# Performance work log

Measured on AMD Instinct MI355X. Metric: run time of the kernel, lower is better.

Reference implementation:

```python
import jax, jax.numpy as jnp
import numpy as np

B, N, H, D, N_HEADS = 8, 2048, 1024, 1, 8
SCALE = H / N_HEADS  # 128.0 ; note: NOT sqrt, faithful to source


def _linear(x, w, b):
    # torch nn.Linear: y = x @ W^T + b ; w: [out, in]
    return jnp.einsum('bnh,oh->bno', x, w) + b


def setup_inputs() -> dict:
    key = jax.random.key(0)
    ks = jax.random.split(key, 18)
    s = 0.02
    inp = {
        'node_t': jax.random.normal(ks[0], (B, N, H), dtype=jnp.float32),
        'node_next': jax.random.normal(ks[1], (B, N, H), dtype=jnp.float32),
        'WQ_w': s * jax.random.normal(ks[2], (H, H), dtype=jnp.float32),
        'WQ_b': s * jax.random.normal(ks[3], (H,), dtype=jnp.float32),
        'WK_w': s * jax.random.normal(ks[4], (H, H), dtype=jnp.float32),
        'WK_b': s * jax.random.normal(ks[5], (H,), dtype=jnp.float32),
        'WV_w': s * jax.random.normal(ks[6], (H, H), dtype=jnp.float32),
        'WV_b': s * jax.random.normal(ks[7], (H,), dtype=jnp.float32),
        'WO_w': s * jax.random.normal(ks[8], (H, H), dtype=jnp.float32),
        'WO_b': s * jax.random.normal(ks[9], (H,), dtype=jnp.float32),
        'WE_w': s * jax.random.normal(ks[10], (H, H), dtype=jnp.float32),
        'WE_b': s * jax.random.normal(ks[11], (H,), dtype=jnp.float32),
        'WN_w': s * jax.random.normal(ks[12], (H, H), dtype=jnp.float32),
        'WN_b': s * jax.random.normal(ks[13], (H,), dtype=jnp.float32),
        'WA_w': s * jax.random.normal(ks[14], (D, H), dtype=jnp.float32),
        'WA_b': s * jax.random.normal(ks[15], (D,), dtype=jnp.float32),
    }
    return inp


def reference(node_t, node_next, WQ_w, WQ_b, WK_w, WK_b, WV_w, WV_b,
              WO_w, WO_b, WE_w, WE_b, WN_w, WN_b, WA_w, WA_b):
    Q = _linear(node_t, WQ_w, WQ_b)       # [B,N,H]
    K = _linear(node_next, WK_w, WK_b)    # [B,N,H]
    V = _linear(node_next, WV_w, WV_b)    # [B,N,H]
    att = jnp.einsum('bih,bkh->bik', Q, K)  # [B,N,N]
    # torch nn.Softmax() with no dim on a 3-D tensor -> legacy dim=0 (batch axis)
    att = jax.nn.softmax(att / SCALE, axis=0)
    # einsum('bnn,bnd->bnd') uses only the diagonal att[b,n,n]
    diag = jnp.einsum('bnn->bn', att)  # [B,N]
    av = diag[:, :, None] * V          # [B,N,H]
    h = jax.nn.gelu(_linear(av, WO_w, WO_b), approximate=False)  # exact erf GELU
    A_t = _linear(node_t, WE_w, WE_b) + _linear(h, WN_w, WN_b)   # [B,N,H]
    A_t = _linear(A_t, WA_w, WA_b)     # [B,N,1]
    return jnp.squeeze(A_t, axis=-1)   # [B,N]
```

## Files before the change

### kernel.cpp

```cpp
#include <hip/hip_runtime.h>
#include <cstdint>
#include <cstddef>


typedef __attribute__((ext_vector_type(8))) short bfx8;
typedef __attribute__((ext_vector_type(4))) short s16x4;
typedef __attribute__((ext_vector_type(4))) float f32x4;

#define N_SEQ 2048
#define M_TOT 16384
#define NT 16

__device__ __forceinline__ unsigned short f2bf(float f) {
  unsigned int u = __float_as_uint(f);
  return (unsigned short)((u + 0x7fffu + ((u >> 16) & 1u)) >> 16);
}
__device__ __forceinline__ float bf2f(short s) {
  return __uint_as_float(((unsigned int)(unsigned short)s) << 16);
}
__device__ __forceinline__ float gelu_exact(float g) {
  return 0.5f * g * (1.0f + erff(g * 0.70710678118654752f));
}
__device__ __forceinline__ void gload16(const void* g, void* l) {
  __builtin_amdgcn_global_load_lds(
      (const __attribute__((address_space(1))) unsigned int*)g,
      (__attribute__((address_space(3))) unsigned int*)(unsigned int)(uintptr_t)l,
      16, 0, 0);
}
__device__ __forceinline__ float blk_sum(float v, float* red, int t) {
#pragma unroll
  for (int o = 32; o > 0; o >>= 1) v += __shfl_down(v, o, 64);
  __syncthreads();
  if ((t & 63) == 0) red[t >> 6] = v;
  __syncthreads();
  return red[0] + red[1] + red[2] + red[3];
}

__global__ __launch_bounds__(256) void colred_kernel(
    const float* __restrict__ WE, const float* __restrict__ WN,
    const float* __restrict__ WQ, const float* __restrict__ WK,
    const float* __restrict__ wa, const float* __restrict__ bQ,
    const float* __restrict__ bK, const float* __restrict__ WEb,
    const float* __restrict__ WNb, const float* __restrict__ WAb,
    float* __restrict__ vE, float* __restrict__ vN,
    float* __restrict__ uQ, float* __restrict__ uK,
    float* __restrict__ c0, float* __restrict__ c1) {
  int y = blockIdx.y;
  if (y < 4) {
    const float* M = y == 0 ? WE : y == 1 ? WN : y == 2 ? WQ : WK;
    const float* wv = (y < 2) ? wa : (y == 2 ? bK : bQ);
    float* dst = y == 0 ? vE : y == 1 ? vN : y == 2 ? uQ : uK;
    int h = blockIdx.x * 256 + threadIdx.x;
    float a = 0.f;
    for (int o = 0; o < 1024; ++o) a += wv[o] * M[(size_t)o * 1024 + h];
    dst[h] = a;
  } else if (blockIdx.x < 2) {
    int t = threadIdx.x;
    float a = 0.f;
    if (blockIdx.x == 0)
      for (int i = t; i < 1024; i += 256) a += wa[i] * (WEb[i] + WNb[i]);
    else
      for (int i = t; i < 1024; i += 256) a += bQ[i] * bK[i];
#pragma unroll
    for (int o = 32; o > 0; o >>= 1) a += __shfl_down(a, o, 64);
    __shared__ float r4[4];
    if ((t & 63) == 0) r4[t >> 6] = a;
    __syncthreads();
    if (t == 0) {
      float tot = r4[0] + r4[1] + r4[2] + r4[3];
      if (blockIdx.x == 0) c0[0] = tot + WAb[0];
      else c1[0] = tot;
    }
  }
}

__global__ __launch_bounds__(256) void rowdot_kernel(
    const float* __restrict__ WO, const float* __restrict__ bV,
    float* __restrict__ bvw) {
  int r = blockIdx.x, t = threadIdx.x;
  __shared__ float red[4];
  float4 wv = ((const float4*)(WO + (size_t)r * 1024))[t];
  float4 bv = ((const float4*)bV)[t];
  float a = wv.x * bv.x + wv.y * bv.y + wv.z * bv.z + wv.w * bv.w;
  float tot = blk_sum(a, red, t);
  if (t == 0) bvw[r] = tot;
}

__global__ __launch_bounds__(256) void cvt_wT_kernel(
    const float* __restrict__ WQ, const float* __restrict__ WK,
    const float* __restrict__ WV, const float* __restrict__ WO,
    short* __restrict__ wqT, short* __restrict__ wkT,
    short* __restrict__ wvT, short* __restrict__ wo) {
  int bi = blockIdx.x, bj = blockIdx.y, z = blockIdx.z, t = threadIdx.x;
  const float* src = z == 0 ? WQ : z == 1 ? WK : z == 2 ? WV : WO;
  if (z == 3) {
#pragma unroll
    for (int i = 0; i < 16; ++i) {
      int lin = i * 256 + t, r = lin >> 6, c = lin & 63;
      size_t idx = (size_t)(bi * 64 + r) * 1024 + bj * 64 + c;
      wo[idx] = (short)f2bf(src[idx]);
    }
    return;
  }
  __shared__ short tile[64][65];
  short* dst = z == 0 ? wqT : z == 1 ? wkT : wvT;
#pragma unroll
  for (int i = 0; i < 16; ++i) {
    int lin = i * 256 + t, r = lin >> 6, c = lin & 63;
    tile[r][c] = (short)f2bf(src[(size_t)(bi * 64 + r) * 1024 + bj * 64 + c]);
  }
  __syncthreads();
#pragma unroll
  for (int i = 0; i < 16; ++i) {
    int lin = i * 256 + t, r = lin >> 6, c = lin & 63;
    dst[(size_t)(bj * 64 + r) * 1024 + bi * 64 + c] = tile[c][r];
  }
}

__global__ __launch_bounds__(128) void cvt_nn_kernel(
    const float* __restrict__ nn, const float* __restrict__ uK,
    short* __restrict__ xn, float* __restrict__ xk) {
  int row = blockIdx.x, t = threadIdx.x;
  const float* src = nn + (size_t)row * 1024 + t * 8;
  float4 v0 = *(const float4*)src;
  float4 v1 = *(const float4*)(src + 4);
  bfx8 o;
  o[0] = (short)f2bf(v0.x); o[1] = (short)f2bf(v0.y);
  o[2] = (short)f2bf(v0.z); o[3] = (short)f2bf(v0.w);
  o[4] = (short)f2bf(v1.x); o[5] = (short)f2bf(v1.y);
  o[6] = (short)f2bf(v1.z); o[7] = (short)f2bf(v1.w);
  *(bfx8*)(xn + (size_t)row * 1024 + t * 8) = o;
  const float4* uv = (const float4*)(uK + t * 8);
  float4 e0 = uv[0], e1 = uv[1];
  float a = v0.x * e0.x + v0.y * e0.y + v0.z * e0.z + v0.w * e0.w +
            v1.x * e1.x + v1.y * e1.y + v1.z * e1.z + v1.w * e1.w;
#pragma unroll
  for (int off = 32; off > 0; off >>= 1) a += __shfl_down(a, off, 64);
  __shared__ float r2[2];
  if ((t & 63) == 0) r2[t >> 6] = a;
  __syncthreads();
  if (t == 0) xk[row] = r2[0] + r2[1];
}

__global__ __launch_bounds__(256) void gemm_pre(
    const short* __restrict__ A0, const short* __restrict__ B0,
    short* __restrict__ D0, const short* __restrict__ A1,
    const short* __restrict__ B1, short* __restrict__ D1) {
  const short* A = blockIdx.z ? A1 : A0;
  const short* B = blockIdx.z ? B1 : B0;
  short* D = blockIdx.z ? D1 : D0;
  __shared__ short sA[128 * 64];
  __shared__ short sB[128 * 64];
  int tid = threadIdx.x, lane = tid & 63, w = tid >> 6;
  int wm = w >> 1, wn = w & 1;
  int bx = blockIdx.x, by = blockIdx.y;
  f32x4 acc[4][4] = {};
  int lrow = lane & 15, lk = (lane >> 4) * 8;
  int srow = lane >> 3, scol = (lane & 7) * 8;
  const short* Ag = A + (size_t)by * 128 * 1024;
  const short* Bg = B + (size_t)bx * 128 * 1024;
  for (int k0 = 0; k0 < 1024; k0 += 64) {
#pragma unroll
    for (int i = 0; i < 4; ++i) {
      int c = w * 4 + i;
      gload16(Ag + (size_t)(c * 8 + srow) * 1024 + k0 + scol, sA + c * 512);
      gload16(Bg + (size_t)(c * 8 + srow) * 1024 + k0 + scol, sB + c * 512);
    }
    __syncthreads();
#pragma unroll
    for (int kk = 0; kk < 64; kk += 32) {
      bfx8 af[4], bfr[4];
#pragma unroll
      for (int mi = 0; mi < 4; ++mi)
        af[mi] = *(const bfx8*)(sA + (wm * 64 + mi * 16 + lrow) * 64 + kk + lk);
#pragma unroll
      for (int nj = 0; nj < 4; ++nj)
        bfr[nj] = *(const bfx8*)(sB + (wn * 64 + nj * 16 + lrow) * 64 + kk + lk);
#pragma unroll
      for (int mi = 0; mi < 4; ++mi)
#pragma unroll
        for (int nj = 0; nj < 4; ++nj)
          acc[mi][nj] = __builtin_amdgcn_mfma_f32_16x16x32_bf16(
              af[mi], bfr[nj], acc[mi][nj], 0, 0, 0);
    }
    __syncthreads();
  }
  int r0 = by * 128 + wm * 64, cb = bx * 128 + wn * 64;
#pragma unroll
  for (int mi = 0; mi < 4; ++mi)
#pragma unroll
    for (int nj = 0; nj < 4; ++nj) {
      int col = cb + nj * 16 + lrow;
#pragma unroll
      for (int r = 0; r < 4; ++r) {
        int row = r0 + mi * 16 + (lane >> 4) * 4 + r;
        D[(size_t)row * 1024 + col] = (short)f2bf(acc[mi][nj][r]);
      }
    }
}

__global__ __launch_bounds__(512, 2) void gemm_main(
    const short* __restrict__ A, const short* __restrict__ Bf,
    const float* __restrict__ bias2, const float* __restrict__ nodet,
    const float* __restrict__ vE, float* __restrict__ sPart,
    float* __restrict__ xePart, short* __restrict__ vw) {
  __shared__ short sA[2][16384];
  __shared__ short sB[2][16384];
  int tid = threadIdx.x;
  int lane = tid & 63, w = tid >> 6;
  int wm = w >> 2, wn = w & 3;
  int wg = blockIdx.x;
  int work = (wg & 7) * 64 + (wg >> 3);
  int by = work >> 3, bx = work & 7;
  int lrow = lane & 15, g = lane >> 4;
  int sw0 = g ^ (lrow & 7);
  int sg = (lane & 7) ^ (lane >> 3);
  const short* Agt = A + ((size_t)(by * 256 + w * 32 + (lane >> 3))) * 1024 + sg * 8;
  const short* Bgt = Bf + ((size_t)(bx * 256 + w * 32 + (lane >> 3))) * 1024 + sg * 8;

  f32x4 acc[8][4] = {};

  auto stage = [&](int buf, int kt) {
    const short* ag = Agt + kt * 64;
    const short* bg = Bgt + kt * 64;
    short* la = &sA[buf][w * 2048];
    short* lb = &sB[buf][w * 2048];
#pragma unroll
    for (int i = 0; i < 4; ++i) {
      gload16(ag + i * 8192, la + i * 512);
      gload16(bg + i * 8192, lb + i * 512);
    }
  };

  stage(0, 0);
  int arow = wm * 128 + lrow;
  int brow = wn * 64 + lrow;
  for (int kt = 0; kt < NT; ++kt) {
    int cur = kt & 1;
    if (kt + 1 < NT) {
      stage(cur ^ 1, kt + 1);
      asm volatile("s_waitcnt vmcnt(8)" ::: "memory");
    } else {
      asm volatile("s_waitcnt vmcnt(0)" ::: "memory");
    }
    __builtin_amdgcn_sched_barrier(0);
    __builtin_amdgcn_s_barrier();
    __builtin_amdgcn_sched_barrier(0);

    const short* sa = &sA[cur][0];
    const short* sb = &sB[cur][0];
    bfx8 bq[4][2];
#pragma unroll
    for (int nj = 0; nj < 4; ++nj) {
      bq[nj][0] = *(const bfx8*)(sb + (brow + nj * 16) * 64 + sw0 * 8);
      bq[nj][1] = *(const bfx8*)(sb + (brow + nj * 16) * 64 + (sw0 ^ 4) * 8);
    }
    bfx8 a0 = *(const bfx8*)(sa + (arow + 0 * 16) * 64 + sw0 * 8);
    bfx8 a1 = *(const bfx8*)(sa + (arow + 0 * 16) * 64 + (sw0 ^ 4) * 8);
    bfx8 a2 = *(const bfx8*)(sa + (arow + 1 * 16) * 64 + sw0 * 8);
    bfx8 a3 = *(const bfx8*)(sa + (arow + 1 * 16) * 64 + (sw0 ^ 4) * 8);
#pragma unroll
    for (int q = 0; q < 4; ++q) {
      bfx8 n0 = a0, n1 = a1, n2 = a2, n3 = a3;
      if (q < 3) {
        n0 = *(const bfx8*)(sa + (arow + (2 * q + 2) * 16) * 64 + sw0 * 8);
        n1 = *(const bfx8*)(sa + (arow + (2 * q + 2) * 16) * 64 + (sw0 ^ 4) * 8);
        n2 = *(const bfx8*)(sa + (arow + (2 * q + 3) * 16) * 64 + sw0 * 8);
        n3 = *(const bfx8*)(sa + (arow + (2 * q + 3) * 16) * 64 + (sw0 ^ 4) * 8);
      }
      __builtin_amdgcn_s_setprio(1);
#pragma unroll
      for (int nj = 0; nj < 4; ++nj) {
        acc[2 * q][nj] = __builtin_amdgcn_mfma_f32_16x16x32_bf16(
            a0, bq[nj][0], acc[2 * q][nj], 0, 0, 0);
        acc[2 * q][nj] = __builtin_amdgcn_mfma_f32_16x16x32_bf16(
            a1, bq[nj][1], acc[2 * q][nj], 0, 0, 0);
        acc[2 * q + 1][nj] = __builtin_amdgcn_mfma_f32_16x16x32_bf16(
            a2, bq[nj][0], acc[2 * q + 1][nj], 0, 0, 0);
        acc[2 * q + 1][nj] = __builtin_amdgcn_mfma_f32_16x16x32_bf16(
            a3, bq[nj][1], acc[2 * q + 1][nj], 0, 0, 0);
      }
      __builtin_amdgcn_s_setprio(0);
      __builtin_amdgcn_sched_barrier(0);
      __builtin_amdgcn_s_barrier();
      __builtin_amdgcn_sched_barrier(0);
      a0 = n0; a1 = n1; a2 = n2; a3 = n3;
    }
  }

  int row0 = by * 256 + wm * 128;
  int cb = bx * 256 + wn * 64;
  if (bx < 4) {
    float bias_nj[4], ve_nj[4];
#pragma unroll
    for (int nj = 0; nj < 4; ++nj) {
      bias_nj[nj] = bias2[cb + nj * 16 + lrow];
      ve_nj[nj] = vE[cb + nj * 16 + lrow];
    }
    int px = bx * 4 + wn;
#pragma unroll
    for (int mi = 0; mi < 8; ++mi) {
#pragma unroll
      for (int r = 0; r < 4; ++r) {
        int row = row0 + mi * 16 + g * 4 + r;
        const float* xr = nodet + (size_t)row * 1024;
        float v = 0.f, v2 = 0.f;
#pragma unroll
        for (int nj = 0; nj < 4; ++nj) {
          float xv = xr[cb + nj * 16 + lrow];
          v += (acc[mi][nj][r] + bias_nj[nj]) * xv;
          v2 += ve_nj[nj] * xv;
        }
        v += __shfl_xor(v, 1, 64);   v2 += __shfl_xor(v2, 1, 64);
        v += __shfl_xor(v, 2, 64);   v2 += __shfl_xor(v2, 2, 64);
        v += __shfl_xor(v, 4, 64);   v2 += __shfl_xor(v2, 4, 64);
        v += __shfl_xor(v, 8, 64);   v2 += __shfl_xor(v2, 8, 64);
        if (lrow == 0) {
          sPart[(size_t)row * 16 + px] = v;
          xePart[(size_t)row * 16 + px] = v2;
        }
      }
    }
  } else {
#pragma unroll
    for (int mi = 0; mi < 8; ++mi)
#pragma unroll
      for (int nj = 0; nj < 4; ++nj) {
        int colv = cb - 1024 + nj * 16 + lrow;
        float bv = bias2[1024 + colv];
#pragma unroll
        for (int r = 0; r < 4; ++r) {
          int row = row0 + mi * 16 + g * 4 + r;
          vw[(size_t)row * 1024 + colv] = (short)f2bf(acc[mi][nj][r] + bv);
        }
      }
  }
}

__global__ __launch_bounds__(64) void sdiag_kernel(
    const float* __restrict__ sPart, const float* __restrict__ xk,
    const float* __restrict__ c1p, float* __restrict__ dg) {
  int n = blockIdx.x, lane = threadIdx.x;
  int b = lane >> 3, j = lane & 7;
  size_t row = (size_t)b * N_SEQ + n;
  float v = sPart[row * 16 + j * 2] + sPart[row * 16 + j * 2 + 1];
  v += __shfl_xor(v, 1, 64);
  v += __shfl_xor(v, 2, 64);
  v += __shfl_xor(v, 4, 64);
  float s = v + xk[row] + c1p[0];
  float m = s;
  m = fmaxf(m, __shfl_xor(m, 8, 64));
  m = fmaxf(m, __shfl_xor(m, 16, 64));
  m = fmaxf(m, __shfl_xor(m, 32, 64));
  float e = expf((s - m) * (1.0f / 128.0f));
  float sum = e;
  sum += __shfl_xor(sum, 8, 64);
  sum += __shfl_xor(sum, 16, 64);
  sum += __shfl_xor(sum, 32, 64);
  if (j == 0) dg[row] = e / sum;
}

__global__ __launch_bounds__(256) void out_kernel(
    const short* __restrict__ vw, const float* __restrict__ dg,
    const float* __restrict__ xePart, const float* __restrict__ vN,
    const float* __restrict__ bO, const float* __restrict__ c0p,
    float* __restrict__ out) {
  int n = blockIdx.x, t = threadIdx.x;
  __shared__ float red[4];
  __shared__ float xeS[8];
  if (t < 128) {
    int b = t >> 4, j = t & 15;
    float p = xePart[((size_t)b * N_SEQ + n) * 16 + j];
    p += __shfl_xor(p, 1, 64);
    p += __shfl_xor(p, 2, 64);
    p += __shfl_xor(p, 4, 64);
    p += __shfl_xor(p, 8, 64);
    if (j == 0) xeS[b] = p;
  }
  __syncthreads();
  float4 bo = ((const float4*)bO)[t];
  float4 vn = ((const float4*)vN)[t];
  float c0 = c0p[0];
#pragma unroll
  for (int b = 0; b < 8; ++b) {
    size_t row = (size_t)b * N_SEQ + n;
    float d = dg[row];
    s16x4 vv = *(const s16x4*)(vw + row * 1024 + t * 4);
    float gx, a = 0.f;
    gx = fmaf(d, bf2f(vv[0]), bo.x); a += gelu_exact(gx) * vn.x;
    gx = fmaf(d, bf2f(vv[1]), bo.y); a += gelu_exact(gx) * vn.y;
    gx = fmaf(d, bf2f(vv[2]), bo.z); a += gelu_exact(gx) * vn.z;
    gx = fmaf(d, bf2f(vv[3]), bo.w); a += gelu_exact(gx) * vn.w;
    float tot = blk_sum(a, red, t);
    if (t == 0) out[row] = xeS[b] + c0 + tot;
  }
}

extern "C" void kernel_launch(void* const* d_in, const int* in_sizes, int n_in,
                              void* d_out, int out_size, void* d_ws,
                              size_t ws_size, hipStream_t stream) {
  const float* nt  = (const float*)d_in[0];
  const float* nn  = (const float*)d_in[1];
  const float* WQ  = (const float*)d_in[2];
  const float* bQ  = (const float*)d_in[3];
  const float* WK  = (const float*)d_in[4];
  const float* bK  = (const float*)d_in[5];
  const float* WV  = (const float*)d_in[6];
  const float* bV  = (const float*)d_in[7];
  const float* WO  = (const float*)d_in[8];
  const float* bO  = (const float*)d_in[9];
  const float* WE  = (const float*)d_in[10];
  const float* WEb = (const float*)d_in[11];
  const float* WN  = (const float*)d_in[12];
  const float* WNb = (const float*)d_in[13];
  const float* wa  = (const float*)d_in[14];
  const float* WAb = (const float*)d_in[15];
  float* out = (float*)d_out;

  char* w = (char*)d_ws;
  size_t o = 0;
  const size_t BIG = (size_t)M_TOT * 1024 * 2;
  short* xn     = (short*)(w + o); o += BIG;
  short* vw     = (short*)(w + o); o += BIG;
  short* Bf     = (short*)(w + o); o += (size_t)2048 * 1024 * 2;
  short* wqT    = (short*)(w + o); o += 2097152;
  short* wkT    = (short*)(w + o); o += 2097152;
  short* wvT    = (short*)(w + o); o += 2097152;
  short* wo     = (short*)(w + o); o += 2097152;
  float* sPart  = (float*)(w + o); o += (size_t)M_TOT * 16 * 4;
  float* xePart = (float*)(w + o); o += (size_t)M_TOT * 16 * 4;
  float* bias2  = (float*)(w + o); o += 8192;
  float* vE     = (float*)(w + o); o += 4096;
  float* vN     = (float*)(w + o); o += 4096;
  float* uK     = (float*)(w + o); o += 4096;
  float* xk     = (float*)(w + o); o += 65536;
  float* dg     = (float*)(w + o); o += 65536;
  float* c0     = (float*)(w + o); o += 256;
  float* c1     = (float*)(w + o); o += 256;
  (void)ws_size; (void)in_sizes; (void)n_in; (void)out_size;

  cvt_wT_kernel<<<dim3(16, 16, 4), 256, 0, stream>>>(WQ, WK, WV, WO,
                                                     wqT, wkT, wvT, wo);
  colred_kernel<<<dim3(4, 5), 256, 0, stream>>>(WE, WN, WQ, WK, wa, bQ, bK,
                                                WEb, WNb, WAb, vE, vN,
                                                bias2, uK, c0, c1);
  rowdot_kernel<<<1024, 256, 0, stream>>>(WO, bV, bias2 + 1024);
  cvt_nn_kernel<<<M_TOT, 128, 0, stream>>>(nn, uK, xn, xk);
  gemm_pre<<<dim3(8, 8, 2), 256, 0, stream>>>(wqT, wkT, Bf,
                                              wo, wvT, Bf + 1048576);
  gemm_main<<<512, 512, 0, stream>>>(xn, Bf, bias2, nt, vE,
                                     sPart, xePart, vw);
  sdiag_kernel<<<N_SEQ, 64, 0, stream>>>(sPart, xk, c1, dg);
  out_kernel<<<N_SEQ, 256, 0, stream>>>(vw, dg, xePart, vN, bO, c0, out);
}
```

Baseline: 180.3 us.

## Triple-buffer A tiles and use one barrier per K step in main GEMM

The A operand gets a three-deep LDS ring, loaded two K-steps ahead, while B stays double-buffered one step ahead. The vmcnt waits are retuned to match the new load ordering. The four per-subtile workgroup barriers inside each K step are replaced by a single barrier at the end of the step, and the A-fragment register prefetch is dropped in favour of direct LDS reads. The aim is to hide more global-load latency and cut synchronisation, at the cost of LDS use growing to 160 KB per block and less overlap of LDS reads with MFMA.

```diff
diff --git a/kernel.cpp b/kernel.cpp
--- a/kernel.cpp
+++ b/kernel.cpp
@@ -204,7 +204,7 @@
     const float* __restrict__ bias2, const float* __restrict__ nodet,
     const float* __restrict__ vE, float* __restrict__ sPart,
     float* __restrict__ xePart, short* __restrict__ vw) {
-  __shared__ short sA[2][16384];
+  __shared__ short sA[3][16384];
   __shared__ short sB[2][16384];
   int tid = threadIdx.x;
   int lane = tid & 63, w = tid >> 6;
@@ -220,54 +220,46 @@
 
   f32x4 acc[8][4] = {};
 
-  auto stage = [&](int buf, int kt) {
-    const short* ag = Agt + kt * 64;
-    const short* bg = Bgt + kt * 64;
-    short* la = &sA[buf][w * 2048];
-    short* lb = &sB[buf][w * 2048];
-#pragma unroll
-    for (int i = 0; i < 4; ++i) {
-      gload16(ag + i * 8192, la + i * 512);
-      gload16(bg + i * 8192, lb + i * 512);
-    }
+  auto stageA = [&](int b, int kt) {
+#pragma unroll
+    for (int i = 0; i < 4; ++i)
+      gload16(Agt + kt * 64 + i * 8192, &sA[b][w * 2048 + i * 512]);
   };
-
-  stage(0, 0);
-  int arow = wm * 128 + lrow;
-  int brow = wn * 64 + lrow;
+  auto stageB = [&](int b, int kt) {
+#pragma unroll
+    for (int i = 0; i < 4; ++i)
+      gload16(Bgt + kt * 64 + i * 8192, &sB[b][w * 2048 + i * 512]);
+  };
+
+  stageA(0, 0);
+  stageB(0, 0);
+  stageA(1, 1);
+
+  int arow = wm * 128 + lrow, brow = wn * 64 + lrow;
   for (int kt = 0; kt < NT; ++kt) {
-    int cur = kt & 1;
-    if (kt + 1 < NT) {
-      stage(cur ^ 1, kt + 1);
-      asm volatile("s_waitcnt vmcnt(8)" ::: "memory");
-    } else {
-      asm volatile("s_waitcnt vmcnt(0)" ::: "memory");
-    }
+    if (kt + 1 < NT) stageB((kt + 1) & 1, kt + 1);
+    if (kt + 2 < NT) stageA((kt + 2) % 3, kt + 2);
+    if (kt < NT - 2)       asm volatile("s_waitcnt vmcnt(12)" ::: "memory");
+    else if (kt == NT - 2) asm volatile("s_waitcnt vmcnt(8)" ::: "memory");
+    else                   asm volatile("s_waitcnt vmcnt(0)" ::: "memory");
     __builtin_amdgcn_sched_barrier(0);
     __builtin_amdgcn_s_barrier();
     __builtin_amdgcn_sched_barrier(0);
 
-    const short* sa = &sA[cur][0];
-    const short* sb = &sB[cur][0];
+    const short* sa = &sA[kt % 3][0];
+    const short* sb = &sB[kt & 1][0];
     bfx8 bq[4][2];
 #pragma unroll
     for (int nj = 0; nj < 4; ++nj) {
       bq[nj][0] = *(const bfx8*)(sb + (brow + nj * 16) * 64 + sw0 * 8);
       bq[nj][1] = *(const bfx8*)(sb + (brow + nj * 16) * 64 + (sw0 ^ 4) * 8);
     }
-    bfx8 a0 = *(const bfx8*)(sa + (arow + 0 * 16) * 64 + sw0 * 8);
-    bfx8 a1 = *(const bfx8*)(sa + (arow + 0 * 16) * 64 + (sw0 ^ 4) * 8);
-    bfx8 a2 = *(const bfx8*)(sa + (arow + 1 * 16) * 64 + sw0 * 8);
-    bfx8 a3 = *(const bfx8*)(sa + (arow + 1 * 16) * 64 + (sw0 ^ 4) * 8);
 #pragma unroll
     for (int q = 0; q < 4; ++q) {
-      bfx8 n0 = a0, n1 = a1, n2 = a2, n3 = a3;
-      if (q < 3) {
-        n0 = *(const bfx8*)(sa + (arow + (2 * q + 2) * 16) * 64 + sw0 * 8);
-        n1 = *(const bfx8*)(sa + (arow + (2 * q + 2) * 16) * 64 + (sw0 ^ 4) * 8);
-        n2 = *(const bfx8*)(sa + (arow + (2 * q + 3) * 16) * 64 + sw0 * 8);
-        n3 = *(const bfx8*)(sa + (arow + (2 * q + 3) * 16) * 64 + (sw0 ^ 4) * 8);
-      }
+      bfx8 a0 = *(const bfx8*)(sa + (arow + (2 * q) * 16) * 64 + sw0 * 8);
+      bfx8 a1 = *(const bfx8*)(sa + (arow + (2 * q) * 16) * 64 + (sw0 ^ 4) * 8);
+      bfx8 a2 = *(const bfx8*)(sa + (arow + (2 * q + 1) * 16) * 64 + sw0 * 8);
+      bfx8 a3 = *(const bfx8*)(sa + (arow + (2 * q + 1) * 16) * 64 + (sw0 ^ 4) * 8);
       __builtin_amdgcn_s_setprio(1);
 #pragma unroll
       for (int nj = 0; nj < 4; ++nj) {
@@ -281,11 +273,10 @@
             a3, bq[nj][1], acc[2 * q + 1][nj], 0, 0, 0);
       }
       __builtin_amdgcn_s_setprio(0);
-      __builtin_amdgcn_sched_barrier(0);
-      __builtin_amdgcn_s_barrier();
-      __builtin_amdgcn_sched_barrier(0);
-      a0 = n0; a1 = n1; a2 = n2; a3 = n3;
-    }
+    }
+    __builtin_amdgcn_sched_barrier(0);
+    __builtin_amdgcn_s_barrier();
+    __builtin_amdgcn_sched_barrier(0);
   }
 
   int row0 = by * 256 + wm * 128;
```

Measured after the change: 200.3 us. 11.1% more time.

## Merge prep kernels into two launches, fuse softmax diag into output kernel

Applied to the files above, without the earlier changes.

Folds the weight conversion, column reductions and row dot into one launch, and the node_next conversion with the small pre-GEMMs into a second launch. The separate batch-axis softmax kernel is folded into the output kernel, so the dg buffer and two launches go away. In the main GEMM, the A-fragment register prefetch is replaced by plain per-step loads, and the per-step barrier is moved to once per k-tile. This cuts launch count and intermediate traffic but may expose LDS latency in the main GEMM.

```diff
diff --git a/kernel.cpp b/kernel.cpp
--- a/kernel.cpp
+++ b/kernel.cpp
@@ -27,133 +27,126 @@
       (__attribute__((address_space(3))) unsigned int*)(unsigned int)(uintptr_t)l,
       16, 0, 0);
 }
-__device__ __forceinline__ float blk_sum(float v, float* red, int t) {
-#pragma unroll
-  for (int o = 32; o > 0; o >>= 1) v += __shfl_down(v, o, 64);
-  __syncthreads();
-  if ((t & 63) == 0) red[t >> 6] = v;
-  __syncthreads();
-  return red[0] + red[1] + red[2] + red[3];
-}
-
-__global__ __launch_bounds__(256) void colred_kernel(
+
+__global__ __launch_bounds__(256) void prep_w(
+    const float* __restrict__ WQ, const float* __restrict__ WK,
+    const float* __restrict__ WV, const float* __restrict__ WO,
     const float* __restrict__ WE, const float* __restrict__ WN,
-    const float* __restrict__ WQ, const float* __restrict__ WK,
     const float* __restrict__ wa, const float* __restrict__ bQ,
-    const float* __restrict__ bK, const float* __restrict__ WEb,
-    const float* __restrict__ WNb, const float* __restrict__ WAb,
+    const float* __restrict__ bK, const float* __restrict__ bV,
+    const float* __restrict__ WEb, const float* __restrict__ WNb,
+    const float* __restrict__ WAb,
+    short* __restrict__ wqT, short* __restrict__ wkT,
+    short* __restrict__ wvT, short* __restrict__ wo_bf,
     float* __restrict__ vE, float* __restrict__ vN,
     float* __restrict__ uQ, float* __restrict__ uK,
-    float* __restrict__ c0, float* __restrict__ c1) {
-  int y = blockIdx.y;
-  if (y < 4) {
+    float* __restrict__ c0, float* __restrict__ c1,
+    float* __restrict__ bvw) {
+  __shared__ short tile[64][65];
+  __shared__ float redw[4];
+  int bid = blockIdx.x, t = threadIdx.x;
+  if (bid < 1024) {
+    int z = bid >> 8, idx = bid & 255, bi = idx >> 4, bj = idx & 15;
+    const float* src = z == 0 ? WQ : z == 1 ? WK : z == 2 ? WV : WO;
+    if (z == 3) {
+#pragma unroll
+      for (int i = 0; i < 16; ++i) {
+        int lin = i * 256 + t, r = lin >> 6, c = lin & 63;
+        size_t idx2 = (size_t)(bi * 64 + r) * 1024 + bj * 64 + c;
+        wo_bf[idx2] = (short)f2bf(src[idx2]);
+      }
+      return;
+    }
+    short* dst = z == 0 ? wqT : z == 1 ? wkT : wvT;
+#pragma unroll
+    for (int i = 0; i < 16; ++i) {
+      int lin = i * 256 + t, r = lin >> 6, c = lin & 63;
+      tile[r][c] = (short)f2bf(src[(size_t)(bi * 64 + r) * 1024 + bj * 64 + c]);
+    }
+    __syncthreads();
+#pragma unroll
+    for (int i = 0; i < 16; ++i) {
+      int lin = i * 256 + t, r = lin >> 6, c = lin & 63;
+      dst[(size_t)(bj * 64 + r) * 1024 + bi * 64 + c] = tile[c][r];
+    }
+  } else if (bid < 1040) {
+    int y = (bid - 1024) >> 2, bx = (bid - 1024) & 3;
     const float* M = y == 0 ? WE : y == 1 ? WN : y == 2 ? WQ : WK;
     const float* wv = (y < 2) ? wa : (y == 2 ? bK : bQ);
     float* dst = y == 0 ? vE : y == 1 ? vN : y == 2 ? uQ : uK;
-    int h = blockIdx.x * 256 + threadIdx.x;
+    int h = bx * 256 + t;
     float a = 0.f;
     for (int o = 0; o < 1024; ++o) a += wv[o] * M[(size_t)o * 1024 + h];
     dst[h] = a;
-  } else if (blockIdx.x < 2) {
-    int t = threadIdx.x;
+  } else if (bid < 1042) {
+    int which = bid - 1040;
     float a = 0.f;
-    if (blockIdx.x == 0)
+    if (which == 0)
       for (int i = t; i < 1024; i += 256) a += wa[i] * (WEb[i] + WNb[i]);
     else
       for (int i = t; i < 1024; i += 256) a += bQ[i] * bK[i];
 #pragma unroll
     for (int o = 32; o > 0; o >>= 1) a += __shfl_down(a, o, 64);
-    __shared__ float r4[4];
-    if ((t & 63) == 0) r4[t >> 6] = a;
+    if ((t & 63) == 0) redw[t >> 6] = a;
     __syncthreads();
     if (t == 0) {
-      float tot = r4[0] + r4[1] + r4[2] + r4[3];
-      if (blockIdx.x == 0) c0[0] = tot + WAb[0];
+      float tot = redw[0] + redw[1] + redw[2] + redw[3];
+      if (which == 0) c0[0] = tot + WAb[0];
       else c1[0] = tot;
     }
-  }
-}
-
-__global__ __launch_bounds__(256) void rowdot_kernel(
-    const float* __restrict__ WO, const float* __restrict__ bV,
-    float* __restrict__ bvw) {
-  int r = blockIdx.x, t = threadIdx.x;
-  __shared__ float red[4];
-  float4 wv = ((const float4*)(WO + (size_t)r * 1024))[t];
-  float4 bv = ((const float4*)bV)[t];
-  float a = wv.x * bv.x + wv.y * bv.y + wv.z * bv.z + wv.w * bv.w;
-  float tot = blk_sum(a, red, t);
-  if (t == 0) bvw[r] = tot;
-}
-
-__global__ __launch_bounds__(256) void cvt_wT_kernel(
-    const float* __restrict__ WQ, const float* __restrict__ WK,
-    const float* __restrict__ WV, const float* __restrict__ WO,
-    short* __restrict__ wqT, short* __restrict__ wkT,
-    short* __restrict__ wvT, short* __restrict__ wo) {
-  int bi = blockIdx.x, bj = blockIdx.y, z = blockIdx.z, t = threadIdx.x;
-  const float* src = z == 0 ? WQ : z == 1 ? WK : z == 2 ? WV : WO;
-  if (z == 3) {
-#pragma unroll
-    for (int i = 0; i < 16; ++i) {
-      int lin = i * 256 + t, r = lin >> 6, c = lin & 63;
-      size_t idx = (size_t)(bi * 64 + r) * 1024 + bj * 64 + c;
-      wo[idx] = (short)f2bf(src[idx]);
-    }
-    return;
-  }
-  __shared__ short tile[64][65];
-  short* dst = z == 0 ? wqT : z == 1 ? wkT : wvT;
-#pragma unroll
-  for (int i = 0; i < 16; ++i) {
-    int lin = i * 256 + t, r = lin >> 6, c = lin & 63;
-    tile[r][c] = (short)f2bf(src[(size_t)(bi * 64 + r) * 1024 + bj * 64 + c]);
-  }
-  __syncthreads();
-#pragma unroll
-  for (int i = 0; i < 16; ++i) {
-    int lin = i * 256 + t, r = lin >> 6, c = lin & 63;
-    dst[(size_t)(bj * 64 + r) * 1024 + bi * 64 + c] = tile[c][r];
-  }
-}
-
-__global__ __launch_bounds__(128) void cvt_nn_kernel(
+  } else {
+    int r = bid - 1042;
+    float4 wv = ((const float4*)(WO + (size_t)r * 1024))[t];
+    float4 bv = ((const float4*)bV)[t];
+    float a = wv.x * bv.x + wv.y * bv.y + wv.z * bv.z + wv.w * bv.w;
+#pragma unroll
+    for (int o = 32; o > 0; o >>= 1) a += __shfl_down(a, o, 64);
+    if ((t & 63) == 0) redw[t >> 6] = a;
+    __syncthreads();
+    if (t == 0) bvw[r] = redw[0] + redw[1] + redw[2] + redw[3];
+  }
+}
+
+__global__ __launch_bounds__(256) void prep2(
+    const short* __restrict__ wqT, const short* __restrict__ wkT,
+    const short* __restrict__ wvT, const short* __restrict__ wo_bf,
+    short* __restrict__ M1, short* __restrict__ M2,
     const float* __restrict__ nn, const float* __restrict__ uK,
     short* __restrict__ xn, float* __restrict__ xk) {
-  int row = blockIdx.x, t = threadIdx.x;
-  const float* src = nn + (size_t)row * 1024 + t * 8;
-  float4 v0 = *(const float4*)src;
-  float4 v1 = *(const float4*)(src + 4);
-  bfx8 o;
-  o[0] = (short)f2bf(v0.x); o[1] = (short)f2bf(v0.y);
-  o[2] = (short)f2bf(v0.z); o[3] = (short)f2bf(v0.w);
-  o[4] = (short)f2bf(v1.x); o[5] = (short)f2bf(v1.y);
-  o[6] = (short)f2bf(v1.z); o[7] = (short)f2bf(v1.w);
-  *(bfx8*)(xn + (size_t)row * 1024 + t * 8) = o;
-  const float4* uv = (const float4*)(uK + t * 8);
-  float4 e0 = uv[0], e1 = uv[1];
-  float a = v0.x * e0.x + v0.y * e0.y + v0.z * e0.z + v0.w * e0.w +
-            v1.x * e1.x + v1.y * e1.y + v1.z * e1.z + v1.w * e1.w;
-#pragma unroll
-  for (int off = 32; off > 0; off >>= 1) a += __shfl_down(a, off, 64);
-  __shared__ float r2[2];
-  if ((t & 63) == 0) r2[t >> 6] = a;
-  __syncthreads();
-  if (t == 0) xk[row] = r2[0] + r2[1];
-}
-
-__global__ __launch_bounds__(256) void gemm_pre(
-    const short* __restrict__ A0, const short* __restrict__ B0,
-    short* __restrict__ D0, const short* __restrict__ A1,
-    const short* __restrict__ B1, short* __restrict__ D1) {
-  const short* A = blockIdx.z ? A1 : A0;
-  const short* B = blockIdx.z ? B1 : B0;
-  short* D = blockIdx.z ? D1 : D0;
   __shared__ short sA[128 * 64];
   __shared__ short sB[128 * 64];
-  int tid = threadIdx.x, lane = tid & 63, w = tid >> 6;
+  __shared__ float red4[4];
+  int bid = blockIdx.x, tid = threadIdx.x;
+  if (bid >= 128) {
+    int cb = bid - 128;
+    int half = tid >> 7, tl = tid & 127;
+    int row = cb * 2 + half;
+    const float* src = nn + (size_t)row * 1024 + tl * 8;
+    float4 v0 = *(const float4*)src;
+    float4 v1 = *(const float4*)(src + 4);
+    bfx8 o;
+    o[0] = (short)f2bf(v0.x); o[1] = (short)f2bf(v0.y);
+    o[2] = (short)f2bf(v0.z); o[3] = (short)f2bf(v0.w);
+    o[4] = (short)f2bf(v1.x); o[5] = (short)f2bf(v1.y);
+    o[6] = (short)f2bf(v1.z); o[7] = (short)f2bf(v1.w);
+    *(bfx8*)(xn + (size_t)row * 1024 + tl * 8) = o;
+    const float4* uv = (const float4*)(uK + tl * 8);
+    float4 e0 = uv[0], e1 = uv[1];
+    float a = v0.x * e0.x + v0.y * e0.y + v0.z * e0.z + v0.w * e0.w +
+              v1.x * e1.x + v1.y * e1.y + v1.z * e1.z + v1.w * e1.w;
+#pragma unroll
+    for (int off = 32; off > 0; off >>= 1) a += __shfl_down(a, off, 64);
+    if ((tid & 63) == 0) red4[tid >> 6] = a;
+    __syncthreads();
+    if (tl == 0) xk[row] = red4[half * 2] + red4[half * 2 + 1];
+    return;
+  }
+  int z = bid >> 6, by = (bid >> 3) & 7, bx = bid & 7;
+  const short* A = z ? wo_bf : wqT;
+  const short* B = z ? wvT : wkT;
+  short* D = z ? M2 : M1;
+  int lane = tid & 63, w = tid >> 6;
   int wm = w >> 1, wn = w & 1;
-  int bx = blockIdx.x, by = blockIdx.y;
   f32x4 acc[4][4] = {};
   int lrow = lane & 15, lk = (lane >> 4) * 8;
   int srow = lane >> 3, scol = (lane & 7) * 8;
@@ -185,12 +178,12 @@
     }
     __syncthreads();
   }
-  int r0 = by * 128 + wm * 64, cb = bx * 128 + wn * 64;
+  int r0 = by * 128 + wm * 64, cb2 = bx * 128 + wn * 64;
 #pragma unroll
   for (int mi = 0; mi < 4; ++mi)
 #pragma unroll
     for (int nj = 0; nj < 4; ++nj) {
-      int col = cb + nj * 16 + lrow;
+      int col = cb2 + nj * 16 + lrow;
 #pragma unroll
       for (int r = 0; r < 4; ++r) {
         int row = r0 + mi * 16 + (lane >> 4) * 4 + r;
@@ -233,10 +226,9 @@
   };
 
   stage(0, 0);
-  int arow = wm * 128 + lrow;
-  int brow = wn * 64 + lrow;
+  int cur = 0;
+  int arow = wm * 128 + lrow, brow = wn * 64 + lrow;
   for (int kt = 0; kt < NT; ++kt) {
-    int cur = kt & 1;
     if (kt + 1 < NT) {
       stage(cur ^ 1, kt + 1);
       asm volatile("s_waitcnt vmcnt(8)" ::: "memory");
@@ -255,19 +247,12 @@
       bq[nj][0] = *(const bfx8*)(sb + (brow + nj * 16) * 64 + sw0 * 8);
       bq[nj][1] = *(const bfx8*)(sb + (brow + nj * 16) * 64 + (sw0 ^ 4) * 8);
     }
-    bfx8 a0 = *(const bfx8*)(sa + (arow + 0 * 16) * 64 + sw0 * 8);
-    bfx8 a1 = *(const bfx8*)(sa + (arow + 0 * 16) * 64 + (sw0 ^ 4) * 8);
-    bfx8 a2 = *(const bfx8*)(sa + (arow + 1 * 16) * 64 + sw0 * 8);
-    bfx8 a3 = *(const bfx8*)(sa + (arow + 1 * 16) * 64 + (sw0 ^ 4) * 8);
 #pragma unroll
     for (int q = 0; q < 4; ++q) {
-      bfx8 n0 = a0, n1 = a1, n2 = a2, n3 = a3;
-      if (q < 3) {
-        n0 = *(const bfx8*)(sa + (arow + (2 * q + 2) * 16) * 64 + sw0 * 8);
-        n1 = *(const bfx8*)(sa + (arow + (2 * q + 2) * 16) * 64 + (sw0 ^ 4) * 8);
-        n2 = *(const bfx8*)(sa + (arow + (2 * q + 3) * 16) * 64 + sw0 * 8);
-        n3 = *(const bfx8*)(sa + (arow + (2 * q + 3) * 16) * 64 + (sw0 ^ 4) * 8);
-      }
+      bfx8 a0 = *(const bfx8*)(sa + (arow + (2 * q) * 16) * 64 + sw0 * 8);
+      bfx8 a1 = *(const bfx8*)(sa + (arow + (2 * q) * 16) * 64 + (sw0 ^ 4) * 8);
+      bfx8 a2 = *(const bfx8*)(sa + (arow + (2 * q + 1) * 16) * 64 + sw0 * 8);
+      bfx8 a3 = *(const bfx8*)(sa + (arow + (2 * q + 1) * 16) * 64 + (sw0 ^ 4) * 8);
       __builtin_amdgcn_s_setprio(1);
 #pragma unroll
       for (int nj = 0; nj < 4; ++nj) {
@@ -281,11 +266,11 @@
             a3, bq[nj][1], acc[2 * q + 1][nj], 0, 0, 0);
       }
       __builtin_amdgcn_s_setprio(0);
-      __builtin_amdgcn_sched_barrier(0);
-      __builtin_amdgcn_s_barrier();
-      __builtin_amdgcn_sched_barrier(0);
-      a0 = n0; a1 = n1; a2 = n2; a3 = n3;
-    }
+    }
+    __builtin_amdgcn_sched_barrier(0);
+    __builtin_amdgcn_s_barrier();
+    __builtin_amdgcn_sched_barrier(0);
+    cur ^= 1;
   }
 
   int row0 = by * 256 + wm * 128;
@@ -337,62 +322,59 @@
   }
 }
 
-__global__ __launch_bounds__(64) void sdiag_kernel(
-    const float* __restrict__ sPart, const float* __restrict__ xk,
-    const float* __restrict__ c1p, float* __restrict__ dg) {
-  int n = blockIdx.x, lane = threadIdx.x;
-  int b = lane >> 3, j = lane & 7;
-  size_t row = (size_t)b * N_SEQ + n;
-  float v = sPart[row * 16 + j * 2] + sPart[row * 16 + j * 2 + 1];
-  v += __shfl_xor(v, 1, 64);
-  v += __shfl_xor(v, 2, 64);
-  v += __shfl_xor(v, 4, 64);
-  float s = v + xk[row] + c1p[0];
-  float m = s;
-  m = fmaxf(m, __shfl_xor(m, 8, 64));
-  m = fmaxf(m, __shfl_xor(m, 16, 64));
-  m = fmaxf(m, __shfl_xor(m, 32, 64));
-  float e = expf((s - m) * (1.0f / 128.0f));
-  float sum = e;
-  sum += __shfl_xor(sum, 8, 64);
-  sum += __shfl_xor(sum, 16, 64);
-  sum += __shfl_xor(sum, 32, 64);
-  if (j == 0) dg[row] = e / sum;
-}
-
-__global__ __launch_bounds__(256) void out_kernel(
-    const short* __restrict__ vw, const float* __restrict__ dg,
-    const float* __restrict__ xePart, const float* __restrict__ vN,
-    const float* __restrict__ bO, const float* __restrict__ c0p,
+__global__ __launch_bounds__(256) void out2_kernel(
+    const short* __restrict__ vw, const float* __restrict__ sPart,
+    const float* __restrict__ xePart, const float* __restrict__ xk,
+    const float* __restrict__ vN, const float* __restrict__ bO,
+    const float* __restrict__ c0p, const float* __restrict__ c1p,
     float* __restrict__ out) {
   int n = blockIdx.x, t = threadIdx.x;
   __shared__ float red[4];
-  __shared__ float xeS[8];
+  __shared__ float sS[8], xeS[8];
   if (t < 128) {
     int b = t >> 4, j = t & 15;
-    float p = xePart[((size_t)b * N_SEQ + n) * 16 + j];
-    p += __shfl_xor(p, 1, 64);
-    p += __shfl_xor(p, 2, 64);
-    p += __shfl_xor(p, 4, 64);
-    p += __shfl_xor(p, 8, 64);
-    if (j == 0) xeS[b] = p;
+    size_t row = (size_t)b * N_SEQ + n;
+    float p = sPart[row * 16 + j];
+    float q = xePart[row * 16 + j];
+    p += __shfl_xor(p, 1, 64);  q += __shfl_xor(q, 1, 64);
+    p += __shfl_xor(p, 2, 64);  q += __shfl_xor(q, 2, 64);
+    p += __shfl_xor(p, 4, 64);  q += __shfl_xor(q, 4, 64);
+    p += __shfl_xor(p, 8, 64);  q += __shfl_xor(q, 8, 64);
+    if (j == 0) {
+      sS[b] = p + xk[row] + c1p[0];
+      xeS[b] = q;
+    }
   }
   __syncthreads();
+  float sv[8], dgv[8];
+#pragma unroll
+  for (int b = 0; b < 8; ++b) sv[b] = sS[b];
+  float m = sv[0];
+#pragma unroll
+  for (int b = 1; b < 8; ++b) m = fmaxf(m, sv[b]);
+  float sum = 0.f;
+#pragma unroll
+  for (int b = 0; b < 8; ++b) { dgv[b] = expf((sv[b] - m) * (1.0f / 128.0f)); sum += dgv[b]; }
+  float inv = 1.0f / sum;
   float4 bo = ((const float4*)bO)[t];
   float4 vn = ((const float4*)vN)[t];
   float c0 = c0p[0];
 #pragma unroll
   for (int b = 0; b < 8; ++b) {
     size_t row = (size_t)b * N_SEQ + n;
-    float d = dg[row];
+    float d = dgv[b] * inv;
     s16x4 vv = *(const s16x4*)(vw + row * 1024 + t * 4);
     float gx, a = 0.f;
     gx = fmaf(d, bf2f(vv[0]), bo.x); a += gelu_exact(gx) * vn.x;
     gx = fmaf(d, bf2f(vv[1]), bo.y); a += gelu_exact(gx) * vn.y;
     gx = fmaf(d, bf2f(vv[2]), bo.z); a += gelu_exact(gx) * vn.z;
     gx = fmaf(d, bf2f(vv[3]), bo.w); a += gelu_exact(gx) * vn.w;
-    float tot = blk_sum(a, red, t);
-    if (t == 0) out[row] = xeS[b] + c0 + tot;
+#pragma unroll
+    for (int o = 32; o > 0; o >>= 1) a += __shfl_down(a, o, 64);
+    __syncthreads();
+    if ((t & 63) == 0) red[t >> 6] = a;
+    __syncthreads();
+    if (t == 0) out[row] = xeS[b] + c0 + red[0] + red[1] + red[2] + red[3];
   }
 }
 
@@ -426,7 +408,7 @@
   short* wqT    = (short*)(w + o); o += 2097152;
   short* wkT    = (short*)(w + o); o += 2097152;
   short* wvT    = (short*)(w + o); o += 2097152;
-  short* wo     = (short*)(w + o); o += 2097152;
+  short* wo_bf  = (short*)(w + o); o += 2097152;
   float* sPart  = (float*)(w + o); o += (size_t)M_TOT * 16 * 4;
   float* xePart = (float*)(w + o); o += (size_t)M_TOT * 16 * 4;
   float* bias2  = (float*)(w + o); o += 8192;
@@ -434,22 +416,17 @@
   float* vN     = (float*)(w + o); o += 4096;
   float* uK     = (float*)(w + o); o += 4096;
   float* xk     = (float*)(w + o); o += 65536;
-  float* dg     = (float*)(w + o); o += 65536;
   float* c0     = (float*)(w + o); o += 256;
   float* c1     = (float*)(w + o); o += 256;
   (void)ws_size; (void)in_sizes; (void)n_in; (void)out_size;
 
-  cvt_wT_kernel<<<dim3(16, 16, 4), 256, 0, stream>>>(WQ, WK, WV, WO,
-                                                     wqT, wkT, wvT, wo);
-  colred_kernel<<<dim3(4, 5), 256, 0, stream>>>(WE, WN, WQ, WK, wa, bQ, bK,
-                                                WEb, WNb, WAb, vE, vN,
-                                                bias2, uK, c0, c1);
-  rowdot_kernel<<<1024, 256, 0, stream>>>(WO, bV, bias2 + 1024);
-  cvt_nn_kernel<<<M_TOT, 128, 0, stream>>>(nn, uK, xn, xk);
-  gemm_pre<<<dim3(8, 8, 2), 256, 0, stream>>>(wqT, wkT, Bf,
-                                              wo, wvT, Bf + 1048576);
+  prep_w<<<2066, 256, 0, stream>>>(WQ, WK, WV, WO, WE, WN, wa, bQ, bK, bV,
+                                   WEb, WNb, WAb, wqT, wkT, wvT, wo_bf,
+                                   vE, vN, bias2, uK, c0, c1, bias2 + 1024);
+  prep2<<<8320, 256, 0, stream>>>(wqT, wkT, wvT, wo_bf, Bf, Bf + 1048576,
+                                  nn, uK, xn, xk);
   gemm_main<<<512, 512, 0, stream>>>(xn, Bf, bias2, nt, vE,
                                      sPart, xePart, vw);
-  sdiag_kernel<<<N_SEQ, 64, 0, stream>>>(sPart, xk, c1, dg);
-  out_kernel<<<N_SEQ, 256, 0, stream>>>(vw, dg, xePart, vN, bO, c0, out);
-}
+  out2_kernel<<<N_SEQ, 256, 0, stream>>>(vw, sPart, xePart, xk, vN, bO,
+                                         c0, c1, out);
+}
```

Measured after the change: 162.8 us. -9.7%, faster.
